# Performance work log

Measured on AMD Instinct MI355X. Metric: run time of the kernel, lower is better.

## Reference

```python
import jax, jax.numpy as jnp
import numpy as np

FRAME_LEN = 128
FFT_LEN = 128            # smallest power of 2 >= frame_length (TF default)
NUM_SPEC_BINS = FFT_LEN // 2 + 1  # 65
NUM_MEL = 80
SAMPLE_RATE = 16000.0
LOWER_HZ, UPPER_HZ = 80.0, 7600.0


def _hz_to_mel(f):
    # TF's HTK-style mel: 1127 * ln(1 + f/700)
    return 1127.0 * np.log1p(np.asarray(f, dtype=np.float64) / 700.0)


def _linear_to_mel_weight_matrix():
    # Faithful port of tf.signal.linear_to_mel_weight_matrix
    linear_freqs = np.linspace(0.0, SAMPLE_RATE / 2.0, NUM_SPEC_BINS)
    spec_mel = _hz_to_mel(linear_freqs[1:])[:, None]            # [64, 1] (bin 0 zeroed)
    edges = np.linspace(_hz_to_mel(LOWER_HZ), _hz_to_mel(UPPER_HZ), NUM_MEL + 2)
    lower, center, upper = edges[None, :-2], edges[None, 1:-1], edges[None, 2:]
    lower_slopes = (spec_mel - lower) / (center - lower)
    upper_slopes = (upper - spec_mel) / (upper - center)
    w = np.maximum(0.0, np.minimum(lower_slopes, upper_slopes))  # [64, 80]
    return np.pad(w, [[1, 0], [0, 0]]).astype(np.float32)        # [65, 80]


_MEL_W = jnp.asarray(_linear_to_mel_weight_matrix())


def setup_inputs() -> dict:
    key = jax.random.key(0)
    x = jax.random.normal(key, (16, 16384), dtype=jnp.float32)
    return {"x": x}


def reference(x):
    B, N = x.shape
    # pad_end=True with frame_step=1 -> N frames, pad FRAME_LEN-1 zeros at the end
    xp = jnp.pad(x, ((0, 0), (0, FRAME_LEN - 1)))
    idx = jnp.arange(N)[:, None] + jnp.arange(FRAME_LEN)[None, :]  # [N, 128]
    frames = xp[:, idx]                                            # [B, N, 128]
    n = jnp.arange(FRAME_LEN, dtype=jnp.float32)
    window = 0.5 - 0.5 * jnp.cos(2.0 * jnp.pi * n / FRAME_LEN)     # periodic Hann
    stft = jnp.fft.rfft(frames * window, n=FFT_LEN, axis=-1)       # [B, N, 65] complex
    mag = jax.lax.stop_gradient(jnp.abs(stft).astype(jnp.float32))
    mel = mag @ _MEL_W                                             # [B, N, 80]
    return jnp.concatenate([x[..., None], mel], axis=-1)           # [B, N, 81]
```

## Files before the change

### kernel.cpp

```cpp
#include <hip/hip_runtime.h>
#include <hip/hip_fp16.h>
#include <math.h>

#define B_SZ 16
#define N_SZ 16384
#define T_FR 64
#define NBIN 65
#define NMEL 80
#define ST   83
#define KN   6


constexpr float QC[33] = {
  1.0f,            0.99879545620f, 0.99518472667f, 0.98917650996f,
  0.98078528040f,  0.97003125319f, 0.95694033573f, 0.94154406518f,
  0.92387953251f,  0.90398929312f, 0.88192126435f, 0.85772861000f,
  0.83146961230f,  0.80320753148f, 0.77301045336f, 0.74095112535f,
  0.70710678119f,  0.67155895485f, 0.63439328416f, 0.59569930449f,
  0.55557023302f,  0.51410274419f, 0.47139673683f, 0.42755509343f,
  0.38268343236f,  0.33688985339f, 0.29028467725f, 0.24298017990f,
  0.19509032202f,  0.14673047446f, 0.09801714033f, 0.04906767433f,
  0.0f
};

__host__ __device__ constexpr float cosi(int k) {
  k = ((k % 128) + 128) % 128;
  return (k <= 32) ? QC[k]
       : (k <= 64) ? -QC[64 - k]
       : (k <= 96) ? -QC[k - 64]
       : QC[128 - k];
}
__host__ __device__ constexpr float sini(int k) { return cosi(k - 32); }
__host__ __device__ constexpr float hannw(int n) { return 0.5f - 0.5f * cosi(n); }
__host__ __device__ constexpr int rev6(int m) {
  return ((m & 1) << 5) | ((m & 2) << 3) | ((m & 4) << 1) |
         ((m & 8) >> 1) | ((m & 16) >> 3) | ((m & 32) >> 5);
}

constexpr double cln(double x) {
  int k = 0;
  while (x > 1.5)  { x *= 0.5; ++k; }
  while (x < 0.75) { x *= 2.0; --k; }
  const double y = (x - 1.0) / (x + 1.0);
  const double y2 = y * y;
  double t = y, s = 0.0;
  for (int i = 0; i < 40; ++i) { s += t / (double)(2 * i + 1); t *= y2; }
  return 2.0 * s + (double)k * 0.69314718055994530942;
}
constexpr double melf(double f) { return 1127.0 * cln(1.0 + f / 700.0); }

struct MelTab {
  int   kbe[NMEL];
  float w[NMEL][KN];
  constexpr MelTab() : kbe{}, w{} {
    const double mlo = melf(80.0), mhi = melf(7600.0);
    const double dm  = (mhi - mlo) / 81.0;
    for (int j = 0; j < NMEL; ++j) {
      const double lower = mlo + dm * (double)j;
      const double upper = lower + 2.0 * dm;
      int kb = 64;
      for (int k = 1; k < NBIN; ++k) {
        const double m = melf(125.0 * (double)k);
        const double a = m - lower, b2 = upper - m;
        if ((a < b2 ? a : b2) > 0.0) { kb = k; break; }
      }
      if (kb > NBIN - KN) kb = NBIN - KN;
      kbe[j] = kb;
      for (int r = 0; r < KN; ++r) {
        const int k = kb + r;
        double ww = 0.0;
        if (k >= 1 && k < NBIN) {
          const double m = melf(125.0 * (double)k);
          const double a = (m - lower) / dm, b2 = (upper - m) / dm;
          ww = a < b2 ? a : b2;
          if (ww < 0.0) ww = 0.0;
        }
        w[j][r] = (float)ww;
      }
    }
  }
};
constexpr MelTab MT{};


template <int LEN>
__device__ __forceinline__ void fft_stage(float (&zr)[64], float (&zi)[64]) {
#pragma unroll
  for (int i = 0; i < 64; i += LEN) {
#pragma unroll
    for (int j = 0; j < LEN / 2; ++j) {
      const int   q  = 128 * j / LEN;
      const float wr = cosi(q);
      const float wi = -sini(q);
      const int   a = i + j, bb = i + j + LEN / 2;
      const float br = zr[bb], bi = zi[bb];
      const float tr = wr * br - wi * bi;
      const float ti = wr * bi + wi * br;
      zr[bb] = zr[a] - tr;
      zi[bb] = zi[a] - ti;
      zr[a] += tr;
      zi[a] += ti;
    }
  }
}

__global__ __launch_bounds__(T_FR) void melspec_kernel(const float* __restrict__ x,
                                                       float* __restrict__ out) {
  __shared__ float  xs[T_FR + 128];
  __shared__ __half stage[T_FR * ST];

  const int tid = threadIdx.x;
  const int t0  = blockIdx.x * T_FR;
  const int b   = blockIdx.y;
  const float* xrow = x + (size_t)b * N_SZ;

  for (int i = tid; i < T_FR + 128; i += T_FR) {
    const int g = t0 + i;
    xs[i] = (g < N_SZ) ? xrow[g] : 0.0f;
  }
  __syncthreads();

  float zr[64], zi[64];
  {
    const float* xf = xs + tid;
#pragma unroll
    for (int m = 0; m < 64; ++m) {
      const int rm = rev6(m);
      zr[m] = xf[2 * rm]     * hannw(2 * rm);
      zi[m] = xf[2 * rm + 1] * hannw(2 * rm + 1);
    }
  }
  fft_stage<2>(zr, zi);
  fft_stage<4>(zr, zi);
  fft_stage<8>(zr, zi);
  fft_stage<16>(zr, zi);
  fft_stage<32>(zr, zi);
  fft_stage<64>(zr, zi);

  float mag[NBIN];
#pragma unroll
  for (int k = 0; k < NBIN; ++k) {
    const int ka = k & 63, kc = (64 - k) & 63;
    const float Ar = zr[ka], Ai = zi[ka];
    const float Br = zr[kc], Bi = zi[kc];
    const float c = cosi(k), s = sini(k);
    const float Xr = (Ar + Br) + c * (Ai + Bi) - s * (Ar - Br);
    const float Xi = (Ai - Bi) - c * (Ar - Br) - s * (Ai + Bi);
    mag[k] = 0.5f * sqrtf(Xr * Xr + Xi * Xi);
  }

  {
    __half* srow = stage + tid * ST;
    srow[0] = __float2half(xs[tid]);
#pragma unroll
    for (int j = 0; j < NMEL; ++j) {
      const int kb = MT.kbe[j];
      float acc = MT.w[j][0] * mag[kb];
#pragma unroll
      for (int r = 1; r < KN; ++r)
        acc = fmaf(MT.w[j][r], mag[kb + r], acc);
      srow[1 + j] = __float2half(acc);
    }
  }

  __syncthreads();

  float* orow = out + ((size_t)b * N_SZ + t0) * 81;
  int t = 0;
  int c = tid;
  for (int i = 0; i < 81; ++i) {
    orow[i * T_FR + tid] = __half2float(stage[t * ST + c]);
    c += T_FR;
    if (c >= 81) { c -= 81; ++t; }
  }
}

extern "C" void kernel_launch(void* const* d_in, const int* in_sizes, int n_in,
                              void* d_out, int out_size, void* d_ws, size_t ws_size,
                              hipStream_t stream) {
  const float* x = (const float*)d_in[0];
  float* out = (float*)d_out;
  dim3 grid(N_SZ / T_FR, B_SZ);
  dim3 block(T_FR);
  hipLaunchKernelGGL(melspec_kernel, grid, block, 0, stream, x, out);
}
```

Baseline: 113.9 us.

## Replace per-thread radix-2 FFT with windowed DFT matrix on MFMA

Replaces the per-thread 128-point register FFT with a direct DFT matmul on MFMA f16 instructions. The Hann-windowed cosine/sine basis is built in shared memory by each block, and four waves each compute 16 frames across 80 padded output bins. Magnitudes go to shared memory as half precision. The mel projection is split across four thread groups, skipping zero weights, and the output is written with float4 stores from an fp32 staging buffer. The aim is to remove heavy register pressure and poor occupancy from the 64-thread FFT blocks. The costs are rebuilding the basis table in every block and accepting f16 precision on inputs and twiddles.

```diff
diff --git a/kernel.cpp b/kernel.cpp
--- a/kernel.cpp
+++ b/kernel.cpp
@@ -5,37 +5,18 @@
 #define B_SZ 16
 #define N_SZ 16384
 #define T_FR 64
+#define NTHR 256
 #define NBIN 65
 #define NMEL 80
-#define ST   83
+#define NCH  81
 #define KN   6
+#define MSTR 70
+#define BSTR 136
 
+typedef _Float16 h8  __attribute__((ext_vector_type(8)));
+typedef float    f4  __attribute__((ext_vector_type(4)));
+static_assert(sizeof(h8) == 16, "h8 must be 4 VGPRs");
 
-constexpr float QC[33] = {
-  1.0f,            0.99879545620f, 0.99518472667f, 0.98917650996f,
-  0.98078528040f,  0.97003125319f, 0.95694033573f, 0.94154406518f,
-  0.92387953251f,  0.90398929312f, 0.88192126435f, 0.85772861000f,
-  0.83146961230f,  0.80320753148f, 0.77301045336f, 0.74095112535f,
-  0.70710678119f,  0.67155895485f, 0.63439328416f, 0.59569930449f,
-  0.55557023302f,  0.51410274419f, 0.47139673683f, 0.42755509343f,
-  0.38268343236f,  0.33688985339f, 0.29028467725f, 0.24298017990f,
-  0.19509032202f,  0.14673047446f, 0.09801714033f, 0.04906767433f,
-  0.0f
-};
-
-__host__ __device__ constexpr float cosi(int k) {
-  k = ((k % 128) + 128) % 128;
-  return (k <= 32) ? QC[k]
-       : (k <= 64) ? -QC[64 - k]
-       : (k <= 96) ? -QC[k - 64]
-       : QC[128 - k];
-}
-__host__ __device__ constexpr float sini(int k) { return cosi(k - 32); }
-__host__ __device__ constexpr float hannw(int n) { return 0.5f - 0.5f * cosi(n); }
-__host__ __device__ constexpr int rev6(int m) {
-  return ((m & 1) << 5) | ((m & 2) << 3) | ((m & 4) << 1) |
-         ((m & 8) >> 1) | ((m & 16) >> 3) | ((m & 32) >> 5);
-}
 
 constexpr double cln(double x) {
   int k = 0;
@@ -82,97 +63,117 @@
 };
 constexpr MelTab MT{};
 
-
-template <int LEN>
-__device__ __forceinline__ void fft_stage(float (&zr)[64], float (&zi)[64]) {
+template <int J0>
+__device__ __forceinline__ void mel20(const __half* mrow, float* srow) {
 #pragma unroll
-  for (int i = 0; i < 64; i += LEN) {
+  for (int jj = 0; jj < 20; ++jj) {
+    const int j = J0 + jj;
+    float acc = 0.0f;
 #pragma unroll
-    for (int j = 0; j < LEN / 2; ++j) {
-      const int   q  = 128 * j / LEN;
-      const float wr = cosi(q);
-      const float wi = -sini(q);
-      const int   a = i + j, bb = i + j + LEN / 2;
-      const float br = zr[bb], bi = zi[bb];
-      const float tr = wr * br - wi * bi;
-      const float ti = wr * bi + wi * br;
-      zr[bb] = zr[a] - tr;
-      zi[bb] = zi[a] - ti;
-      zr[a] += tr;
-      zi[a] += ti;
+    for (int r = 0; r < KN; ++r) {
+      if (MT.w[j][r] != 0.0f)
+        acc = fmaf(MT.w[j][r], __half2float(mrow[MT.kbe[j] + r]), acc);
     }
+    srow[1 + j] = acc;
   }
 }
 
-__global__ __launch_bounds__(T_FR) void melspec_kernel(const float* __restrict__ x,
-                                                       float* __restrict__ out) {
-  __shared__ float  xs[T_FR + 128];
-  __shared__ __half stage[T_FR * ST];
+__global__ __launch_bounds__(NTHR, 3) void melspec_kernel(const float* __restrict__ x,
+                                                          float* __restrict__ out) {
+  __shared__ __align__(16) unsigned char smem[160 * BSTR * 2];
+  __shared__ float  xs[192];
+  __shared__ __half magh[T_FR * MSTR];
 
   const int tid = threadIdx.x;
   const int t0  = blockIdx.x * T_FR;
   const int b   = blockIdx.y;
+
   const float* xrow = x + (size_t)b * N_SZ;
+  if (tid < 192) xs[tid] = (t0 + tid < N_SZ) ? xrow[t0 + tid] : 0.0f;
 
-  for (int i = tid; i < T_FR + 128; i += T_FR) {
-    const int g = t0 + i;
-    xs[i] = (g < N_SZ) ? xrow[g] : 0.0f;
+  {
+    _Float16* bt = (_Float16*)smem;
+    const float w0 = 6.2831853071795864769f / 128.0f;
+    for (int e = tid; e < NBIN * 128; e += NTHR) {
+      const int k = e >> 7, n = e & 127;
+      const float wh = 0.5f - 0.5f * __cosf(w0 * (float)n);
+      float sv, cv;
+      __sincosf(w0 * (float)((k * n) & 127), &sv, &cv);
+      bt[k * BSTR + n]        = (_Float16)(wh * cv);
+      bt[(80 + k) * BSTR + n] = (_Float16)(-wh * sv);
+    }
+    for (int e = tid; e < 15 * 128; e += NTHR) {
+      const int c = e >> 7, n = e & 127;
+      bt[(65 + c) * BSTR + n]  = (_Float16)0.f;
+      bt[(145 + c) * BSTR + n] = (_Float16)0.f;
+    }
   }
   __syncthreads();
 
-  float zr[64], zi[64];
+  const int wv = tid >> 6;
+  const int ln = tid & 63;
+  const int lr = ln & 15;
+  const int lg = ln >> 4;
+
+  f4 acc[10];
   {
-    const float* xf = xs + tid;
+    const f4 z = {0.f, 0.f, 0.f, 0.f};
 #pragma unroll
-    for (int m = 0; m < 64; ++m) {
-      const int rm = rev6(m);
-      zr[m] = xf[2 * rm]     * hannw(2 * rm);
-      zi[m] = xf[2 * rm + 1] * hannw(2 * rm + 1);
+    for (int i = 0; i < 10; ++i) acc[i] = z;
+  }
+
+  const _Float16* btp = (const _Float16*)smem;
+#pragma unroll
+  for (int kk = 0; kk < 4; ++kk) {
+    h8 a;
+    const float* ap = xs + 16 * wv + lr + kk * 32 + lg * 8;
+#pragma unroll
+    for (int j = 0; j < 8; ++j) a[j] = (_Float16)ap[j];
+    h8 bfr[10];
+#pragma unroll
+    for (int nt = 0; nt < 10; ++nt)
+      bfr[nt] = *(const h8*)(btp + (nt * 16 + lr) * BSTR + kk * 32 + lg * 8);
+#pragma unroll
+    for (int nt = 0; nt < 10; ++nt)
+      acc[nt] = __builtin_amdgcn_mfma_f32_16x16x32_f16(a, bfr[nt], acc[nt], 0, 0, 0);
+  }
+
+#pragma unroll
+  for (int r = 0; r < 5; ++r) {
+    if (r < 4 || lr == 0) {
+      const int k = r * 16 + lr;
+#pragma unroll
+      for (int v = 0; v < 4; ++v) {
+        const int t = 16 * wv + lg * 4 + v;
+        const float re = acc[r][v], im = acc[r + 5][v];
+        magh[t * MSTR + k] = __float2half(sqrtf(re * re + im * im));
+      }
     }
   }
-  fft_stage<2>(zr, zi);
-  fft_stage<4>(zr, zi);
-  fft_stage<8>(zr, zi);
-  fft_stage<16>(zr, zi);
-  fft_stage<32>(zr, zi);
-  fft_stage<64>(zr, zi);
+  __syncthreads();
 
-  float mag[NBIN];
-#pragma unroll
-  for (int k = 0; k < NBIN; ++k) {
-    const int ka = k & 63, kc = (64 - k) & 63;
-    const float Ar = zr[ka], Ai = zi[ka];
-    const float Br = zr[kc], Bi = zi[kc];
-    const float c = cosi(k), s = sini(k);
-    const float Xr = (Ar + Br) + c * (Ai + Bi) - s * (Ar - Br);
-    const float Xi = (Ai - Bi) - c * (Ar - Br) - s * (Ai + Bi);
-    mag[k] = 0.5f * sqrtf(Xr * Xr + Xi * Xi);
-  }
-
+  float* stage = (float*)smem;
   {
-    __half* srow = stage + tid * ST;
-    srow[0] = __float2half(xs[tid]);
-#pragma unroll
-    for (int j = 0; j < NMEL; ++j) {
-      const int kb = MT.kbe[j];
-      float acc = MT.w[j][0] * mag[kb];
-#pragma unroll
-      for (int r = 1; r < KN; ++r)
-        acc = fmaf(MT.w[j][r], mag[kb + r], acc);
-      srow[1 + j] = __float2half(acc);
+    const int t = tid & 63, q = tid >> 6;
+    const __half* mrow = magh + t * MSTR;
+    float* srow = stage + t * NCH;
+    if (q == 0) srow[0] = xs[t];
+    switch (q) {
+      case 0:  mel20<0>(mrow, srow);  break;
+      case 1:  mel20<20>(mrow, srow); break;
+      case 2:  mel20<40>(mrow, srow); break;
+      default: mel20<60>(mrow, srow); break;
     }
   }
-
   __syncthreads();
 
-  float* orow = out + ((size_t)b * N_SZ + t0) * 81;
-  int t = 0;
-  int c = tid;
-  for (int i = 0; i < 81; ++i) {
-    orow[i * T_FR + tid] = __half2float(stage[t * ST + c]);
-    c += T_FR;
-    if (c >= 81) { c -= 81; ++t; }
+  float* orow = out + ((size_t)b * N_SZ + t0) * NCH;
+#pragma unroll
+  for (int i = 0; i < 5; ++i) {
+    const int f = i * 1024 + tid * 4;
+    *(float4*)(orow + f) = *(const float4*)(stage + f);
   }
+  if (tid < 64) orow[5120 + tid] = stage[5120 + tid];
 }
 
 extern "C" void kernel_launch(void* const* d_in, const int* in_sizes, int n_in,
@@ -181,6 +182,6 @@
   const float* x = (const float*)d_in[0];
   float* out = (float*)d_out;
   dim3 grid(N_SZ / T_FR, B_SZ);
-  dim3 block(T_FR);
+  dim3 block(NTHR);
   hipLaunchKernelGGL(melspec_kernel, grid, block, 0, stream, x, out);
 }
```

After: 120.0 us. 5.4% more time.
